# Kernel tuning notes

Hardware: AMD Instinct MI355X
Metric: run time of the kernel (lower is better)

Reference implementation:

```python
import jax, jax.numpy as jnp
import numpy as np

B, N, C, H = 4, 8192, 1024, 16
D = C // H

def setup_inputs() -> dict:
    key = jax.random.key(0)
    k1, k2, k3 = jax.random.split(key, 3)
    scale_in = 1.0 / np.sqrt(C)
    return {
        "x": jax.random.normal(k1, (B, N, C), dtype=jnp.float32),
        "w_qkv": jax.random.normal(k2, (C, 3 * C), dtype=jnp.float32) * scale_in,
        "b_qkv": jnp.zeros((3 * C,), dtype=jnp.float32),
        "w_proj": jax.random.normal(k3, (C, C), dtype=jnp.float32) * scale_in,
        "b_proj": jnp.zeros((C,), dtype=jnp.float32),
    }

def reference(x, w_qkv, b_qkv, w_proj, b_proj):
    Bx, Nx, Cx = x.shape
    qkv = x @ w_qkv + b_qkv                       # [B,N,3C]
    qkv = qkv.reshape(Bx, Nx, 3, H, D)
    qkv = jnp.transpose(qkv, (2, 0, 3, 1, 4))     # [3,B,H,N,D]
    q, k, v = qkv[0], qkv[1], qkv[2]
    q = jax.nn.elu(q) + 1.0                       # positive feature map
    k = jax.nn.elu(k) + 1.0
    kv = jnp.einsum('bhnd,bhne->bhde', k, v)      # [B,H,D,D]
    out = jnp.einsum('bhnd,bhde->bhne', q, kv)    # [B,H,N,D]
    z = 1.0 / (jnp.einsum('bhnd,bhd->bhn', q, k.sum(axis=2)) + 1e-8)
    out = out * z[..., None]
    out = jnp.transpose(out, (0, 2, 1, 3)).reshape(Bx, Nx, Cx)
    out = out @ w_proj + b_proj                   # dropout is identity in eval
    return out
```

## Files before the change

kernel.cpp:

```cpp
#include <hip/hip_runtime.h>
#include <hip/hip_bf16.h>
#include <stdint.h>

typedef unsigned short ushort_t;
typedef __attribute__((ext_vector_type(8))) short short8;
typedef __attribute__((ext_vector_type(4))) float floatx4;

__device__ __forceinline__ ushort_t f2b(float f) {
    unsigned u = __float_as_uint(f);
    unsigned r = (u + 0x7FFFu + ((u >> 16) & 1u)) >> 16;
    return (ushort_t)r;
}
__device__ __forceinline__ float b2f(ushort_t h) {
    return __uint_as_float(((unsigned)h) << 16);
}
__device__ __forceinline__ float elu1(float f) {
    return (f > 0.f) ? (f + 1.f) : __expf(f);
}

#define GLDS16(srcp, dstp)                                                          \
    __builtin_amdgcn_global_load_lds(                                               \
        (const __attribute__((address_space(1))) unsigned int*)(srcp),              \
        (__attribute__((address_space(3))) unsigned int*)(dstp), 16, 0, 0)


__global__ void conv_bf16(const float* __restrict__ in, ushort_t* __restrict__ out, int n8) {
    for (int i = blockIdx.x * blockDim.x + threadIdx.x; i < n8; i += gridDim.x * blockDim.x) {
        const float4 f0 = *(const float4*)&in[(size_t)i * 8];
        const float4 f1 = *(const float4*)&in[(size_t)i * 8 + 4];
        ushort4 o0, o1;
        o0.x = f2b(f0.x); o0.y = f2b(f0.y); o0.z = f2b(f0.z); o0.w = f2b(f0.w);
        o1.x = f2b(f1.x); o1.y = f2b(f1.y); o1.z = f2b(f1.z); o1.w = f2b(f1.w);
        *(ushort4*)&out[(size_t)i * 8]     = o0;
        *(ushort4*)&out[(size_t)i * 8 + 4] = o1;
    }
}

__global__ void transpose_conv(const float* __restrict__ in, ushort_t* __restrict__ out,
                               int R, int C) {
    __shared__ float tile[32][33];
    int c0 = blockIdx.x * 32, r0 = blockIdx.y * 32;
    int tx = threadIdx.x, ty = threadIdx.y;
#pragma unroll
    for (int k = 0; k < 4; ++k) {
        int a = ty * 4 + k;
        tile[a][tx] = in[(size_t)(r0 + a) * C + c0 + tx];
    }
    __syncthreads();
#pragma unroll
    for (int k = 0; k < 4; ++k) {
        int a = ty * 4 + k;
        out[(size_t)(c0 + a) * R + r0 + tx] = f2b(tile[tx][a]);
    }
}

__global__ void zero_f32(float* __restrict__ p, int n) {
    int i = blockIdx.x * blockDim.x + threadIdx.x;
    if (i < n) p[i] = 0.f;
}

template<int MODE>
__global__ __launch_bounds__(512, 2) void gemm256(
    const ushort_t* __restrict__ A, const ushort_t* __restrict__ Bt,
    const float* __restrict__ bias,
    ushort_t* __restrict__ out_u16, float* __restrict__ out_f32,
    int Nt, int nbx, int nt)
{
    extern __shared__ ushort_t lds[];
    constexpr int KK = 1024;

    const int tid  = threadIdx.x;
    const int wave = tid >> 6;
    const int lane = tid & 63;
    const int wm_i = wave >> 2;
    const int wn_i = wave & 3;
    const int fr   = lane & 15;
    const int fq   = lane >> 4;

    const int bid  = (int)blockIdx.x;
    const int bswz = ((bid & 7) << 5) + (bid >> 3);
    const int ntiles = nt << 8;

    const int trow = tid >> 3;
    const int csw  = ((tid & 7) ^ (trow & 7)) << 3;
    const int tcolB = ((tid >> 8) << 6) + (trow & 31);

    const int dstA = wave * 512;
    const int dstB = 16384 + wave * 512;

    const int sw0 = (fq ^ (fr & 7)) << 3;
    const int sw1 = sw0 ^ 32;
    const int abase = (wm_i * 64 + fr) * 64;
    const int bbase = (wn_i * 32 + fr) * 64;
    int loA0[2][2], loA1[2][2], loB0[2][2], loB1[2][2];
#pragma unroll
    for (int bf = 0; bf < 2; ++bf)
#pragma unroll
        for (int q = 0; q < 2; ++q) {
            loA0[bf][q] = bf * 32768 + q * 8192 + abase + sw0;
            loA1[bf][q] = bf * 32768 + q * 8192 + abase + sw1;
            loB0[bf][q] = bf * 32768 + 16384 + q * 8192 + bbase + sw0;
            loB1[bf][q] = bf * 32768 + 16384 + q * 8192 + bbase + sw1;
        }

    floatx4 acc[8][4];
    const floatx4 z4 = {0.f, 0.f, 0.f, 0.f};
#pragma unroll
    for (int i = 0; i < 8; ++i)
#pragma unroll
        for (int j = 0; j < 4; ++j) acc[i][j] = z4;

    short8 a[4][2], b[2][2];

    auto tilebase = [&](int t, const ushort_t*& sA, const ushort_t*& sB, int& mm, int& nn) {
        const int byy = t / nbx;
        const int bxx = t - byy * nbx;
        mm = byy << 8; nn = bxx << 8;
        sA = A  + (size_t)(mm + trow)  * KK + csw;
        sB = Bt + (size_t)(nn + tcolB) * KK + csw;
    };

    auto stageA = [&](const ushort_t* sp, int buf, int h, int ko) {
        ushort_t* d = lds + buf * 32768 + h * 8192 + dstA;
        GLDS16(sp + h * (64 * KK) + ko, d);
        GLDS16(sp + h * (64 * KK) + 128 * KK + ko, d + 4096);
    };
    auto stageB = [&](const ushort_t* sp, int buf, int h, int ko) {
        ushort_t* d = lds + buf * 32768 + h * 8192 + dstB;
        GLDS16(sp + h * (32 * KK) + ko, d);
        GLDS16(sp + h * (32 * KK) + 128 * KK + ko, d + 4096);
    };
    auto loadA = [&](int buf, int qr) {
        const int o0 = loA0[buf][qr], o1 = loA1[buf][qr];
#pragma unroll
        for (int i = 0; i < 4; ++i) {
            a[i][0] = *(const short8*)(lds + o0 + i * 1024);
            a[i][1] = *(const short8*)(lds + o1 + i * 1024);
        }
    };
    auto loadB = [&](int buf, int qc) {
        const int o0 = loB0[buf][qc], o1 = loB1[buf][qc];
#pragma unroll
        for (int j = 0; j < 2; ++j) {
            b[j][0] = *(const short8*)(lds + o0 + j * 1024);
            b[j][1] = *(const short8*)(lds + o1 + j * 1024);
        }
    };
    auto mma = [&](int qr, int qc) {
#pragma unroll
        for (int i = 0; i < 4; ++i)
#pragma unroll
            for (int j = 0; j < 2; ++j) {
                acc[qr * 4 + i][qc * 2 + j] =
                    __builtin_amdgcn_mfma_f32_16x16x32_bf16(b[j][0], a[i][0], acc[qr * 4 + i][qc * 2 + j], 0, 0, 0);
                acc[qr * 4 + i][qc * 2 + j] =
                    __builtin_amdgcn_mfma_f32_16x16x32_bf16(b[j][1], a[i][1], acc[qr * 4 + i][qc * 2 + j], 0, 0, 0);
            }
    };

    auto epilogue = [&](int m0, int n0) {
        float4 bv[4];
#pragma unroll
        for (int cj = 0; cj < 4; ++cj) {
            const int nb = n0 + wn_i * 64 + (cj >> 1) * 32 + (cj & 1) * 16 + fq * 4;
            bv[cj] = *(const float4*)&bias[nb];
        }
#pragma unroll
        for (int ri = 0; ri < 8; ++ri) {
            const int m = m0 + wm_i * 128 + (ri >> 2) * 64 + (ri & 3) * 16 + fr;
#pragma unroll
            for (int cj = 0; cj < 4; ++cj) {
                const int col = n0 + wn_i * 64 + (cj >> 1) * 32 + (cj & 1) * 16 + fq * 4;
                float v0 = acc[ri][cj][0] + bv[cj].x;
                float v1 = acc[ri][cj][1] + bv[cj].y;
                float v2 = acc[ri][cj][2] + bv[cj].z;
                float v3 = acc[ri][cj][3] + bv[cj].w;
                if (MODE == 0) {
                    const int s  = col >> 10;
                    const int c  = col & 1023;
                    const int h  = c >> 6;
                    const int d  = c & 63;
                    const int bb = m >> 13;
                    const int n  = m & 8191;
                    if (s < 2) { v0 = elu1(v0); v1 = elu1(v1); v2 = elu1(v2); v3 = elu1(v3); }
                    ushort4 o;
                    o.x = f2b(v0); o.y = f2b(v1); o.z = f2b(v2); o.w = f2b(v3);
                    *(ushort4*)&out_u16[(((size_t)s * 64 + bb * 16 + h) * 8192 + n) * 64 + d] = o;
                } else {
                    float4 o; o.x = v0; o.y = v1; o.z = v2; o.w = v3;
                    *(float4*)&out_f32[(size_t)m * Nt + col] = o;
                }
            }
        }
    };

#define PRIO1() __builtin_amdgcn_s_setprio(1)
#define BOUT()  __builtin_amdgcn_s_setprio(0); __builtin_amdgcn_s_barrier()
#define VM6()   asm volatile("s_waitcnt vmcnt(6)" ::: "memory")

    const ushort_t *saC, *sbC, *saN, *sbN;
    int m0, n0, m0N, n0N;
    int tC = bswz;
    tilebase(tC, saC, sbC, m0, n0);
    int tN = (tC + 256 < ntiles) ? tC + 256 : tC;
    tilebase(tN, saN, sbN, m0N, n0N);

    stageA(saC, 0, 0, 0);
    stageB(sbC, 0, 1, 0);
    stageA(saC, 0, 1, 0);
    stageB(sbC, 0, 0, 0);
    stageA(saC, 1, 0, 64);
    stageB(sbC, 1, 1, 64);
    stageA(saC, 1, 1, 64);
    VM6();
    __builtin_amdgcn_s_barrier();

    for (int ot = 0; ot < nt; ++ot) {
        int ko = 0;
        for (int pr = 0; pr < 7; ++pr, ko += 128) {
            loadA(0, 0); loadB(0, 0);
            stageB(sbC, 1, 0, ko + 64);
            PRIO1(); mma(0, 0); BOUT();

            loadB(0, 1);
            stageA(saC, 0, 0, ko + 128);
            PRIO1(); mma(0, 1); BOUT();

            loadA(0, 1);
            stageB(sbC, 0, 1, ko + 128);
            PRIO1(); mma(1, 1); BOUT();

            loadB(0, 0);
            stageA(saC, 0, 1, ko + 128);
            PRIO1(); mma(1, 0); __builtin_amdgcn_s_setprio(0); VM6();
            __builtin_amdgcn_s_barrier();

            loadA(1, 0); loadB(1, 0);
            stageB(sbC, 0, 0, ko + 128);
            PRIO1(); mma(0, 0); BOUT();

            loadB(1, 1);
            stageA(saC, 1, 0, ko + 192);
            PRIO1(); mma(0, 1); BOUT();

            loadA(1, 1);
            stageB(sbC, 1, 1, ko + 192);
            PRIO1(); mma(1, 1); BOUT();

            loadB(1, 0);
            stageA(saC, 1, 1, ko + 192);
            PRIO1(); mma(1, 0); __builtin_amdgcn_s_setprio(0); VM6();
            __builtin_amdgcn_s_barrier();
        }

        loadA(0, 0); loadB(0, 0);
        stageB(sbC, 1, 0, 960);
        PRIO1(); mma(0, 0); BOUT();

        loadB(0, 1);
        stageA(saN, 0, 0, 0);
        PRIO1(); mma(0, 1); BOUT();

        loadA(0, 1);
        stageB(sbN, 0, 1, 0);
        PRIO1(); mma(1, 1); BOUT();

        loadB(0, 0);
        stageA(saN, 0, 1, 0);
        PRIO1(); mma(1, 0); __builtin_amdgcn_s_setprio(0); VM6();
        __builtin_amdgcn_s_barrier();

        loadA(1, 0); loadB(1, 0);
        stageB(sbN, 0, 0, 0);
        PRIO1(); mma(0, 0); BOUT();

        loadB(1, 1);
        stageA(saN, 1, 0, 64);
        PRIO1(); mma(0, 1); BOUT();

        loadA(1, 1);
        stageB(sbN, 1, 1, 64);
        PRIO1(); mma(1, 1); BOUT();

        loadB(1, 0);
        stageA(saN, 1, 1, 64);
        PRIO1(); mma(1, 0); __builtin_amdgcn_s_setprio(0); VM6();
        __builtin_amdgcn_s_barrier();

        epilogue(m0, n0);
#pragma unroll
        for (int i = 0; i < 8; ++i)
#pragma unroll
            for (int j = 0; j < 4; ++j) acc[i][j] = z4;

        saC = saN; sbC = sbN; m0 = m0N; n0 = n0N; tC = tN;
        tN = (tC + 256 < ntiles) ? tC + 256 : tC;
        tilebase(tN, saN, sbN, m0N, n0N);
    }

#undef PRIO1
#undef BOUT
#undef VM6
}

__global__ __launch_bounds__(256) void kv_kernel(
    const ushort_t* __restrict__ kbuf, const ushort_t* __restrict__ vbuf,
    float* __restrict__ kv, float* __restrict__ ksum)
{
    __shared__ ushort_t ks[64 * 64] __attribute__((aligned(16)));
    __shared__ ushort_t vs[64 * 64] __attribute__((aligned(16)));

    const int bh = blockIdx.y, chunk = blockIdx.x, t = threadIdx.x;
    const int d0 = (t >> 4) * 4, e0 = (t & 15) * 4;
    const bool do_ksum = (t & 15) == 0;

    float acc[4][4];
#pragma unroll
    for (int i = 0; i < 4; ++i)
#pragma unroll
        for (int j = 0; j < 4; ++j) acc[i][j] = 0.f;
    float kacc[4] = {0.f, 0.f, 0.f, 0.f};

    for (int sub = 0; sub < 8; ++sub) {
        const int nb = chunk * 512 + sub * 64;
        __syncthreads();
#pragma unroll
        for (int p = 0; p < 2; ++p) {
            int idx = p * 256 + t;
            int r = idx >> 3, c = (idx & 7) * 8;
            *(short8*)&ks[r * 64 + c] = *(const short8*)&kbuf[((size_t)bh * 8192 + nb + r) * 64 + c];
            *(short8*)&vs[r * 64 + c] = *(const short8*)&vbuf[((size_t)bh * 8192 + nb + r) * 64 + c];
        }
        __syncthreads();
        for (int n = 0; n < 64; ++n) {
            ushort4 kd = *(const ushort4*)&ks[n * 64 + d0];
            ushort4 ve = *(const ushort4*)&vs[n * 64 + e0];
            float kf[4] = {b2f(kd.x), b2f(kd.y), b2f(kd.z), b2f(kd.w)};
            float vf[4] = {b2f(ve.x), b2f(ve.y), b2f(ve.z), b2f(ve.w)};
#pragma unroll
            for (int i = 0; i < 4; ++i) {
#pragma unroll
                for (int j = 0; j < 4; ++j) acc[i][j] += kf[i] * vf[j];
            }
            if (do_ksum) {
#pragma unroll
                for (int i = 0; i < 4; ++i) kacc[i] += kf[i];
            }
        }
    }
#pragma unroll
    for (int i = 0; i < 4; ++i) {
        if (do_ksum) atomicAdd(&ksum[bh * 64 + d0 + i], kacc[i]);
#pragma unroll
        for (int j = 0; j < 4; ++j)
            atomicAdd(&kv[((size_t)bh * 64 + d0 + i) * 64 + e0 + j], acc[i][j]);
    }
}

__global__ __launch_bounds__(256) void out_kernel(
    const ushort_t* __restrict__ qbuf, const float* __restrict__ kv,
    const float* __restrict__ ksum, ushort_t* __restrict__ obuf)
{
    __shared__ float kvs[4096];
    __shared__ float ksums[64];

    const int bh = blockIdx.y, chunk = blockIdx.x, t = threadIdx.x;
    const int b = bh >> 4, h = bh & 15;
    const int wave = t >> 6, lane = t & 63;
    const int tok = lane & 15, fq = lane >> 4;

#pragma unroll
    for (int i = 0; i < 4; ++i) {
        int idx = (i * 256 + t) * 4;
        *(float4*)&kvs[idx] = *(const float4*)&kv[(size_t)bh * 4096 + idx];
    }
    if (t < 64) ksums[t] = ksum[bh * 64 + t];
    __syncthreads();

    short8 afr[4][2];
#pragma unroll
    for (int et = 0; et < 4; ++et)
#pragma unroll
        for (int kslice = 0; kslice < 2; ++kslice)
#pragma unroll
            for (int i = 0; i < 8; ++i) {
                const int d = kslice * 32 + fq * 8 + i;
                afr[et][kslice][i] = (short)f2b(kvs[d * 64 + et * 16 + tok]);
            }
    short8 zfr[2];
#pragma unroll
    for (int kslice = 0; kslice < 2; ++kslice)
#pragma unroll
        for (int i = 0; i < 8; ++i)
            zfr[kslice][i] = (short)f2b(ksums[kslice * 32 + fq * 8 + i]);

    const floatx4 z4 = {0.f, 0.f, 0.f, 0.f};
    const int nbase = chunk * 1024 + wave * 256;
    const ushort_t* qrow = qbuf + ((size_t)bh * 8192 + nbase + tok) * 64 + fq * 8;
    ushort_t* orow = obuf + ((size_t)b * 8192 + nbase + tok) * 1024 + h * 64 + fq * 4;

#pragma unroll 2
    for (int g = 0; g < 16; ++g) {
        short8 bf0 = *(const short8*)(qrow + (size_t)g * 16 * 64);
        short8 bf1 = *(const short8*)(qrow + (size_t)g * 16 * 64 + 32);

        floatx4 az = __builtin_amdgcn_mfma_f32_16x16x32_bf16(zfr[0], bf0, z4, 0, 0, 0);
        az = __builtin_amdgcn_mfma_f32_16x16x32_bf16(zfr[1], bf1, az, 0, 0, 0);

        floatx4 ad[4];
#pragma unroll
        for (int et = 0; et < 4; ++et) {
            ad[et] = __builtin_amdgcn_mfma_f32_16x16x32_bf16(afr[et][0], bf0, z4, 0, 0, 0);
            ad[et] = __builtin_amdgcn_mfma_f32_16x16x32_bf16(afr[et][1], bf1, ad[et], 0, 0, 0);
        }

        const float zi = 1.f / (az[0] + 1e-8f);
#pragma unroll
        for (int et = 0; et < 4; ++et) {
            ushort4 o;
            o.x = f2b(ad[et][0] * zi);
            o.y = f2b(ad[et][1] * zi);
            o.z = f2b(ad[et][2] * zi);
            o.w = f2b(ad[et][3] * zi);
            *(ushort4*)&orow[(size_t)g * 16 * 1024 + et * 16] = o;
        }
    }
}


extern "C" void kernel_launch(void* const* d_in, const int* in_sizes, int n_in,
                              void* d_out, int out_size, void* d_ws, size_t ws_size,
                              hipStream_t stream) {
    const float* x      = (const float*)d_in[0];
    const float* w_qkv  = (const float*)d_in[1];
    const float* b_qkv  = (const float*)d_in[2];
    const float* w_proj = (const float*)d_in[3];
    const float* b_proj = (const float*)d_in[4];
    float* out = (float*)d_out;

    const size_t XE = (size_t)32768 * 1024;

    char* ws = (char*)d_ws;
    ushort_t* xb   = (ushort_t*)ws;  ws += XE * 2;
    ushort_t* wqT  = (ushort_t*)ws;  ws += (size_t)3072 * 1024 * 2;
    ushort_t* wpT  = (ushort_t*)ws;  ws += (size_t)1024 * 1024 * 2;
    ushort_t* qkvb = (ushort_t*)ws;  ws += 3 * XE * 2;
    ushort_t* ob   = (ushort_t*)ws;  ws += XE * 2;
    float*    kv   = (float*)ws;     ws += (size_t)64 * 64 * 64 * 4;
    float*    ksum = (float*)ws;     ws += (size_t)64 * 64 * 4;

    (void)hipFuncSetAttribute(reinterpret_cast<const void*>(gemm256<0>),
                              hipFuncAttributeMaxDynamicSharedMemorySize, 131072);
    (void)hipFuncSetAttribute(reinterpret_cast<const void*>(gemm256<1>),
                              hipFuncAttributeMaxDynamicSharedMemorySize, 131072);

    zero_f32<<<dim3((64 * 64 * 64 + 64 * 64 + 255) / 256), dim3(256), 0, stream>>>(kv, 64 * 64 * 64 + 64 * 64);
    conv_bf16<<<dim3(2048), dim3(256), 0, stream>>>(x, xb, (int)(XE / 8));
    transpose_conv<<<dim3(96, 32), dim3(32, 8), 0, stream>>>(w_qkv, wqT, 1024, 3072);
    transpose_conv<<<dim3(32, 32), dim3(32, 8), 0, stream>>>(w_proj, wpT, 1024, 1024);

    gemm256<0><<<dim3(256), dim3(512), 131072, stream>>>(xb, wqT, b_qkv, qkvb, nullptr, 3072, 12, 6);

    kv_kernel<<<dim3(16, 64), dim3(256), 0, stream>>>(qkvb + XE, qkvb + 2 * XE, kv, ksum);
    out_kernel<<<dim3(8, 64), dim3(256), 0, stream>>>(qkvb, kv, ksum, ob);

    gemm256<1><<<dim3(256), dim3(512), 131072, stream>>>(ob, wpT, b_proj, nullptr, out, 1024, 4, 2);
}
```

Baseline: 475.2 us.

## Compute K^T V and key sums with MFMA using transposed LDS reads

Replaces the scalar FMA kv_kernel with a matrix-core version. Each wave stages its own 64-token K and V slab in LDS, reads it with ds_read_b64_tr_b16 transpose loads, and accumulates K^T V with 16x16x32 bf16 MFMAs. The key sum is an extra MFMA against a vector of ones. Per-wave partials are reduced in LDS before the global atomics, and the grid is halved so each block covers 1024 tokens. The aim is to move the reduction off slow scalar FP32 FMAs and to cut the number of atomics, at the cost of relying on the inline-asm transpose read and a custom swizzled layout.

```diff
diff --git a/kernel.cpp b/kernel.cpp
--- a/kernel.cpp
+++ b/kernel.cpp
@@ -4,6 +4,7 @@
 
 typedef unsigned short ushort_t;
 typedef __attribute__((ext_vector_type(8))) short short8;
+typedef __attribute__((ext_vector_type(4))) short short4v;
 typedef __attribute__((ext_vector_type(4))) float floatx4;
 
 __device__ __forceinline__ ushort_t f2b(float f) {
@@ -22,6 +23,14 @@
     __builtin_amdgcn_global_load_lds(                                               \
         (const __attribute__((address_space(1))) unsigned int*)(srcp),              \
         (__attribute__((address_space(3))) unsigned int*)(dstp), 16, 0, 0)
+
+__device__ __forceinline__ short4v tr16(const ushort_t* p) {
+    short4v r;
+    const __attribute__((address_space(3))) ushort_t* p3 =
+        (const __attribute__((address_space(3))) ushort_t*)p;
+    asm volatile("ds_read_b64_tr_b16 %0, %1" : "=v"(r) : "v"(p3));
+    return r;
+}
 
 
 __global__ void conv_bf16(const float* __restrict__ in, ushort_t* __restrict__ out, int n8) {
@@ -303,57 +312,116 @@
 #undef VM6
 }
 
-__global__ __launch_bounds__(256) void kv_kernel(
+__global__ __launch_bounds__(256) void kvg2_kernel(
     const ushort_t* __restrict__ kbuf, const ushort_t* __restrict__ vbuf,
     float* __restrict__ kv, float* __restrict__ ksum)
 {
-    __shared__ ushort_t ks[64 * 64] __attribute__((aligned(16)));
-    __shared__ ushort_t vs[64 * 64] __attribute__((aligned(16)));
+    __shared__ ushort_t stg[4][2][4096] __attribute__((aligned(16)));
+    __shared__ float ksr[4][64];
 
     const int bh = blockIdx.y, chunk = blockIdx.x, t = threadIdx.x;
-    const int d0 = (t >> 4) * 4, e0 = (t & 15) * 4;
-    const bool do_ksum = (t & 15) == 0;
-
-    float acc[4][4];
-#pragma unroll
-    for (int i = 0; i < 4; ++i)
-#pragma unroll
-        for (int j = 0; j < 4; ++j) acc[i][j] = 0.f;
-    float kacc[4] = {0.f, 0.f, 0.f, 0.f};
-
-    for (int sub = 0; sub < 8; ++sub) {
-        const int nb = chunk * 512 + sub * 64;
-        __syncthreads();
-#pragma unroll
-        for (int p = 0; p < 2; ++p) {
-            int idx = p * 256 + t;
-            int r = idx >> 3, c = (idx & 7) * 8;
-            *(short8*)&ks[r * 64 + c] = *(const short8*)&kbuf[((size_t)bh * 8192 + nb + r) * 64 + c];
-            *(short8*)&vs[r * 64 + c] = *(const short8*)&vbuf[((size_t)bh * 8192 + nb + r) * 64 + c];
-        }
-        __syncthreads();
-        for (int n = 0; n < 64; ++n) {
-            ushort4 kd = *(const ushort4*)&ks[n * 64 + d0];
-            ushort4 ve = *(const ushort4*)&vs[n * 64 + e0];
-            float kf[4] = {b2f(kd.x), b2f(kd.y), b2f(kd.z), b2f(kd.w)};
-            float vf[4] = {b2f(ve.x), b2f(ve.y), b2f(ve.z), b2f(ve.w)};
-#pragma unroll
-            for (int i = 0; i < 4; ++i) {
-#pragma unroll
-                for (int j = 0; j < 4; ++j) acc[i][j] += kf[i] * vf[j];
+    const int wave = t >> 6, lane = t & 63;
+    const int fr = lane & 15, fq = lane >> 4;
+
+    const int srow = lane >> 3;
+    const int dcp  = lane & 7;
+    const int woff = (dcp >> 1) * 1024 + srow * 16 + (dcp & 1) * 8;
+
+    const int troff = fq * 256 + fr * 8;
+
+    short8 ones;
+#pragma unroll
+    for (int i = 0; i < 8; ++i) ones[i] = (short)0x3F80;
+
+    floatx4 av[4][4], ak[4];
+    const floatx4 z4 = {0.f, 0.f, 0.f, 0.f};
+#pragma unroll
+    for (int i = 0; i < 4; ++i) {
+        ak[i] = z4;
+#pragma unroll
+        for (int j = 0; j < 4; ++j) av[i][j] = z4;
+    }
+
+    const size_t rowbase = (size_t)bh * 8192;
+    ushort_t* kreg = &stg[wave][0][0];
+    ushort_t* vreg = &stg[wave][1][0];
+
+#pragma unroll 1
+    for (int s2 = 0; s2 < 4; ++s2) {
+        const int n0 = chunk * 1024 + wave * 256 + s2 * 64;
+#pragma unroll
+        for (int g = 0; g < 8; ++g) {
+            const int n = g * 8 + srow;
+            const size_t src = (rowbase + n0 + n) * 64 + dcp * 8;
+            *(short8*)&kreg[woff + g * 128] = *(const short8*)&kbuf[src];
+            *(short8*)&vreg[woff + g * 128] = *(const short8*)&vbuf[src];
+        }
+        asm volatile("s_waitcnt lgkmcnt(0)" ::: "memory");
+        __builtin_amdgcn_sched_barrier(0);
+
+#pragma unroll
+        for (int ns = 0; ns < 2; ++ns) {
+            short8 ka[4], vb[4];
+#pragma unroll
+            for (int dt = 0; dt < 4; ++dt) {
+                const ushort_t* kb = kreg + dt * 1024 + ns * 512;
+                short4v lo = tr16((const ushort_t*)((const char*)kb + troff));
+                short4v hi = tr16((const ushort_t*)((const char*)kb + troff + 128));
+                ka[dt] = __builtin_shufflevector(lo, hi, 0, 1, 2, 3, 4, 5, 6, 7);
             }
-            if (do_ksum) {
-#pragma unroll
-                for (int i = 0; i < 4; ++i) kacc[i] += kf[i];
+#pragma unroll
+            for (int et = 0; et < 4; ++et) {
+                const ushort_t* vB = vreg + et * 1024 + ns * 512;
+                short4v lo = tr16((const ushort_t*)((const char*)vB + troff));
+                short4v hi = tr16((const ushort_t*)((const char*)vB + troff + 128));
+                vb[et] = __builtin_shufflevector(lo, hi, 0, 1, 2, 3, 4, 5, 6, 7);
             }
-        }
-    }
-#pragma unroll
-    for (int i = 0; i < 4; ++i) {
-        if (do_ksum) atomicAdd(&ksum[bh * 64 + d0 + i], kacc[i]);
-#pragma unroll
-        for (int j = 0; j < 4; ++j)
-            atomicAdd(&kv[((size_t)bh * 64 + d0 + i) * 64 + e0 + j], acc[i][j]);
+            asm volatile("s_waitcnt lgkmcnt(0)" ::: "memory");
+            __builtin_amdgcn_sched_barrier(0);
+
+#pragma unroll
+            for (int dt = 0; dt < 4; ++dt) {
+                ak[dt] = __builtin_amdgcn_mfma_f32_16x16x32_bf16(ka[dt], ones, ak[dt], 0, 0, 0);
+#pragma unroll
+                for (int et = 0; et < 4; ++et)
+                    av[dt][et] = __builtin_amdgcn_mfma_f32_16x16x32_bf16(ka[dt], vb[et], av[dt][et], 0, 0, 0);
+            }
+        }
+    }
+
+    float* red = (float*)&stg[wave][0][0];
+#pragma unroll
+    for (int dt = 0; dt < 4; ++dt)
+#pragma unroll
+        for (int et = 0; et < 4; ++et)
+#pragma unroll
+            for (int r = 0; r < 4; ++r)
+                red[(dt * 16 + fq * 4 + r) * 64 + et * 16 + fr] = av[dt][et][r];
+    if (fr == 0) {
+#pragma unroll
+        for (int dt = 0; dt < 4; ++dt)
+#pragma unroll
+            for (int r = 0; r < 4; ++r)
+                ksr[wave][dt * 16 + fq * 4 + r] = ak[dt][r];
+    }
+    __syncthreads();
+
+    const float* base = (const float*)&stg[0][0][0];
+#pragma unroll
+    for (int j = 0; j < 4; ++j) {
+        const int idx = t * 16 + j * 4;
+        float4 s0 = *(const float4*)&base[0 * 4096 + idx];
+        float4 s1 = *(const float4*)&base[1 * 4096 + idx];
+        float4 s2 = *(const float4*)&base[2 * 4096 + idx];
+        float4 s3 = *(const float4*)&base[3 * 4096 + idx];
+        atomicAdd(&kv[(size_t)bh * 4096 + idx + 0], s0.x + s1.x + s2.x + s3.x);
+        atomicAdd(&kv[(size_t)bh * 4096 + idx + 1], s0.y + s1.y + s2.y + s3.y);
+        atomicAdd(&kv[(size_t)bh * 4096 + idx + 2], s0.z + s1.z + s2.z + s3.z);
+        atomicAdd(&kv[(size_t)bh * 4096 + idx + 3], s0.w + s1.w + s2.w + s3.w);
+    }
+    if (t < 64) {
+        float s = ksr[0][t] + ksr[1][t] + ksr[2][t] + ksr[3][t];
+        atomicAdd(&ksum[bh * 64 + t], s);
     }
 }
 
@@ -461,7 +529,7 @@
 
     gemm256<0><<<dim3(256), dim3(512), 131072, stream>>>(xb, wqT, b_qkv, qkvb, nullptr, 3072, 12, 6);
 
-    kv_kernel<<<dim3(16, 64), dim3(256), 0, stream>>>(qkvb + XE, qkvb + 2 * XE, kv, ksum);
+    kvg2_kernel<<<dim3(8, 64), dim3(256), 0, stream>>>(qkvb + XE, qkvb + 2 * XE, kv, ksum);
     out_kernel<<<dim3(8, 64), dim3(256), 0, stream>>>(qkvb, kv, ksum, ob);
 
     gemm256<1><<<dim3(256), dim3(512), 131072, stream>>>(ob, wpT, b_proj, nullptr, out, 1024, 4, 2);
```

After: 486.9 us. 2.4% more time.

## Fuse prep kernels into one launch and remap GEMM tiles per XCD for L2 locality

Applied to the files above, without the earlier changes.

Merges the zeroing, x conversion and two weight transpose-convert kernels into a single block-partitioned prep kernel, removing three launches. It also replaces the persistent GEMM tile order with a per-XCD mapping. Each group of blocks sharing bid&7 now covers a contiguous rectangle of output tiles, so its A and B panels stay in that die's L2. The risk is uneven work across the prep branches, and the tile mapping depends on how blocks are assigned to XCDs.

```diff
diff --git a/kernel.cpp b/kernel.cpp
--- a/kernel.cpp
+++ b/kernel.cpp
@@ -23,40 +23,56 @@
         (const __attribute__((address_space(1))) unsigned int*)(srcp),              \
         (__attribute__((address_space(3))) unsigned int*)(dstp), 16, 0, 0)
 
-
-__global__ void conv_bf16(const float* __restrict__ in, ushort_t* __restrict__ out, int n8) {
-    for (int i = blockIdx.x * blockDim.x + threadIdx.x; i < n8; i += gridDim.x * blockDim.x) {
-        const float4 f0 = *(const float4*)&in[(size_t)i * 8];
-        const float4 f1 = *(const float4*)&in[(size_t)i * 8 + 4];
-        ushort4 o0, o1;
-        o0.x = f2b(f0.x); o0.y = f2b(f0.y); o0.z = f2b(f0.z); o0.w = f2b(f0.w);
-        o1.x = f2b(f1.x); o1.y = f2b(f1.y); o1.z = f2b(f1.z); o1.w = f2b(f1.w);
-        *(ushort4*)&out[(size_t)i * 8]     = o0;
-        *(ushort4*)&out[(size_t)i * 8 + 4] = o1;
-    }
-}
-
-__global__ void transpose_conv(const float* __restrict__ in, ushort_t* __restrict__ out,
-                               int R, int C) {
+__global__ __launch_bounds__(256) void prep_kernel(
+    const float* __restrict__ x, const float* __restrict__ wq, const float* __restrict__ wp,
+    ushort_t* __restrict__ xb, ushort_t* __restrict__ wqT, ushort_t* __restrict__ wpT,
+    float* __restrict__ kvz)
+{
     __shared__ float tile[32][33];
-    int c0 = blockIdx.x * 32, r0 = blockIdx.y * 32;
-    int tx = threadIdx.x, ty = threadIdx.y;
-#pragma unroll
-    for (int k = 0; k < 4; ++k) {
-        int a = ty * 4 + k;
-        tile[a][tx] = in[(size_t)(r0 + a) * C + c0 + tx];
-    }
-    __syncthreads();
-#pragma unroll
-    for (int k = 0; k < 4; ++k) {
-        int a = ty * 4 + k;
-        out[(size_t)(c0 + a) * R + r0 + tx] = f2b(tile[tx][a]);
-    }
-}
-
-__global__ void zero_f32(float* __restrict__ p, int n) {
-    int i = blockIdx.x * blockDim.x + threadIdx.x;
-    if (i < n) p[i] = 0.f;
+    const int bid = blockIdx.x;
+    const int t = threadIdx.x;
+    const int tx = t & 31, ty = t >> 5;
+
+    if (bid < 3072) {
+        const int c0 = (bid % 96) * 32, r0 = (bid / 96) * 32;
+#pragma unroll
+        for (int k = 0; k < 4; ++k) {
+            int a = ty * 4 + k;
+            tile[a][tx] = wq[(size_t)(r0 + a) * 3072 + c0 + tx];
+        }
+        __syncthreads();
+#pragma unroll
+        for (int k = 0; k < 4; ++k) {
+            int a = ty * 4 + k;
+            wqT[(size_t)(c0 + a) * 1024 + r0 + tx] = f2b(tile[tx][a]);
+        }
+    } else if (bid < 4096) {
+        const int b2 = bid - 3072;
+        const int c0 = (b2 & 31) * 32, r0 = (b2 >> 5) * 32;
+#pragma unroll
+        for (int k = 0; k < 4; ++k) {
+            int a = ty * 4 + k;
+            tile[a][tx] = wp[(size_t)(r0 + a) * 1024 + c0 + tx];
+        }
+        __syncthreads();
+#pragma unroll
+        for (int k = 0; k < 4; ++k) {
+            int a = ty * 4 + k;
+            wpT[(size_t)(c0 + a) * 1024 + r0 + tx] = f2b(tile[tx][a]);
+        }
+    } else if (bid < 5120) {
+        for (int i = (bid - 4096) * 256 + t; i < 4194304; i += 1024 * 256) {
+            const float4 f0 = *(const float4*)&x[(size_t)i * 8];
+            const float4 f1 = *(const float4*)&x[(size_t)i * 8 + 4];
+            ushort4 o0, o1;
+            o0.x = f2b(f0.x); o0.y = f2b(f0.y); o0.z = f2b(f0.z); o0.w = f2b(f0.w);
+            o1.x = f2b(f1.x); o1.y = f2b(f1.y); o1.z = f2b(f1.z); o1.w = f2b(f1.w);
+            *(ushort4*)&xb[(size_t)i * 8]     = o0;
+            *(ushort4*)&xb[(size_t)i * 8 + 4] = o1;
+        }
+    } else {
+        for (int i = (bid - 5120) * 256 + t; i < 266240; i += 128 * 256) kvz[i] = 0.f;
+    }
 }
 
 template<int MODE>
@@ -64,7 +80,7 @@
     const ushort_t* __restrict__ A, const ushort_t* __restrict__ Bt,
     const float* __restrict__ bias,
     ushort_t* __restrict__ out_u16, float* __restrict__ out_f32,
-    int Nt, int nbx, int nt)
+    int Nt, int nt)
 {
     extern __shared__ ushort_t lds[];
     constexpr int KK = 1024;
@@ -78,8 +94,6 @@
     const int fq   = lane >> 4;
 
     const int bid  = (int)blockIdx.x;
-    const int bswz = ((bid & 7) << 5) + (bid >> 3);
-    const int ntiles = nt << 8;
 
     const int trow = tid >> 3;
     const int csw  = ((tid & 7) ^ (trow & 7)) << 3;
@@ -112,7 +126,22 @@
 
     short8 a[4][2], b[2][2];
 
+    auto tile_of = [&](int ot) -> int {
+        const int x = bid & 7, lid = bid >> 3;
+        const int tl = ot * 32 + lid;
+        if (MODE == 0) {
+            const int row = ((x >> 1) << 5) + tl / 6;
+            const int col = (x & 1) * 6 + (tl % 6);
+            return row * 12 + col;
+        } else {
+            const int row = (x << 4) + (tl >> 2);
+            const int col = tl & 3;
+            return row * 4 + col;
+        }
+    };
+
     auto tilebase = [&](int t, const ushort_t*& sA, const ushort_t*& sB, int& mm, int& nn) {
+        const int nbx = (MODE == 0) ? 12 : 4;
         const int byy = t / nbx;
         const int bxx = t - byy * nbx;
         mm = byy << 8; nn = bxx << 8;
@@ -200,10 +229,8 @@
 
     const ushort_t *saC, *sbC, *saN, *sbN;
     int m0, n0, m0N, n0N;
-    int tC = bswz;
-    tilebase(tC, saC, sbC, m0, n0);
-    int tN = (tC + 256 < ntiles) ? tC + 256 : tC;
-    tilebase(tN, saN, sbN, m0N, n0N);
+    tilebase(tile_of(0), saC, sbC, m0, n0);
+    tilebase(tile_of(nt > 1 ? 1 : 0), saN, sbN, m0N, n0N);
 
     stageA(saC, 0, 0, 0);
     stageB(sbC, 0, 1, 0);
@@ -293,9 +320,9 @@
 #pragma unroll
             for (int j = 0; j < 4; ++j) acc[i][j] = z4;
 
-        saC = saN; sbC = sbN; m0 = m0N; n0 = n0N; tC = tN;
-        tN = (tC + 256 < ntiles) ? tC + 256 : tC;
-        tilebase(tN, saN, sbN, m0N, n0N);
+        saC = saN; sbC = sbN; m0 = m0N; n0 = n0N;
+        const int nxt = (ot + 2 < nt) ? ot + 2 : nt - 1;
+        tilebase(tile_of(nxt), saN, sbN, m0N, n0N);
     }
 
 #undef PRIO1
@@ -454,15 +481,12 @@
     (void)hipFuncSetAttribute(reinterpret_cast<const void*>(gemm256<1>),
                               hipFuncAttributeMaxDynamicSharedMemorySize, 131072);
 
-    zero_f32<<<dim3((64 * 64 * 64 + 64 * 64 + 255) / 256), dim3(256), 0, stream>>>(kv, 64 * 64 * 64 + 64 * 64);
-    conv_bf16<<<dim3(2048), dim3(256), 0, stream>>>(x, xb, (int)(XE / 8));
-    transpose_conv<<<dim3(96, 32), dim3(32, 8), 0, stream>>>(w_qkv, wqT, 1024, 3072);
-    transpose_conv<<<dim3(32, 32), dim3(32, 8), 0, stream>>>(w_proj, wpT, 1024, 1024);
-
-    gemm256<0><<<dim3(256), dim3(512), 131072, stream>>>(xb, wqT, b_qkv, qkvb, nullptr, 3072, 12, 6);
+    prep_kernel<<<dim3(5248), dim3(256), 0, stream>>>(x, w_qkv, w_proj, xb, wqT, wpT, kv);
+
+    gemm256<0><<<dim3(256), dim3(512), 131072, stream>>>(xb, wqT, b_qkv, qkvb, nullptr, 3072, 6);
 
     kv_kernel<<<dim3(16, 64), dim3(256), 0, stream>>>(qkvb + XE, qkvb + 2 * XE, kv, ksum);
     out_kernel<<<dim3(8, 64), dim3(256), 0, stream>>>(qkvb, kv, ksum, ob);
 
-    gemm256<1><<<dim3(256), dim3(512), 131072, stream>>>(ob, wpT, b_proj, nullptr, out, 1024, 4, 2);
-}
+    gemm256<1><<<dim3(256), dim3(512), 131072, stream>>>(ob, wpT, b_proj, nullptr, out, 1024, 2);
+}
```

Result: slower. 527.7 us (+11.0%).
